# Kernel optimization log

Hardware: AMD Instinct MI355X
Metric: run time of the kernel (lower is better)

## Reference

```python
import jax, jax.numpy as jnp
import numpy as np

DIM = 16
HEADS = 2
EPS = 1e-5


def _layer_norm(x, g, b):
    m = x.mean(-1, keepdims=True)
    v = ((x - m) ** 2).mean(-1, keepdims=True)
    return (x - m) * jax.lax.rsqrt(v + EPS) * g + b


def setup_inputs() -> dict:
    key = jax.random.key(0)
    ks = jax.random.split(key, 8)
    B, Lq, Lk, D = 4, 2048, 2048, DIM
    xavier = float(np.sqrt(6.0 / (D + D)))  # xavier_uniform bound for square Linear
    inp = {
        "query": jax.random.normal(ks[0], (B, Lq, D), jnp.float32),
        "key": jax.random.normal(ks[1], (B, Lk, D), jnp.float32),
        "value": jax.random.normal(ks[2], (B, Lk, D), jnp.float32),
        "w": jax.random.normal(ks[3], (B, HEADS, Lq, Lk), jnp.float32) * 0.1,
        "mask": jnp.zeros((B, HEADS, Lq, Lk), jnp.float32),
        # LayerNorm params (q, k, v)
        "ln_qg": jnp.ones((D,), jnp.float32), "ln_qb": jnp.zeros((D,), jnp.float32),
        "ln_kg": jnp.ones((D,), jnp.float32), "ln_kb": jnp.zeros((D,), jnp.float32),
        "ln_vg": jnp.ones((D,), jnp.float32), "ln_vb": jnp.zeros((D,), jnp.float32),
        # Linear projections, torch layout [out, in]
        "Wq": jax.random.uniform(ks[4], (D, D), jnp.float32, -xavier, xavier),
        "bq": jnp.zeros((D,), jnp.float32),
        "Wk": jax.random.uniform(ks[5], (D, D), jnp.float32, -xavier, xavier),
        "bk": jnp.zeros((D,), jnp.float32),
        "Wv": jax.random.uniform(ks[6], (D, D), jnp.float32, -xavier, xavier),
        "bv": jnp.zeros((D,), jnp.float32),
        "Wo": jax.random.normal(ks[7], (D, D), jnp.float32) * (1.0 / np.sqrt(D)),
        "bo": jnp.zeros((D,), jnp.float32),
    }
    return inp


def reference(query, key, value, w, mask,
              ln_qg, ln_qb, ln_kg, ln_kb, ln_vg, ln_vb,
              Wq, bq, Wk, bk, Wv, bv, Wo, bo):
    B, Lq, D = query.shape
    H = HEADS
    dh = D // H
    q = _layer_norm(query, ln_qg, ln_qb)
    k = _layer_norm(key, ln_kg, ln_kb)
    v = _layer_norm(value, ln_vg, ln_vb)
    q0 = q  # residual is post-LayerNorm query
    # torch Linear: x @ W.T + b ; split heads -> [B, H, L, dh]
    Q = (q @ Wq.T + bq).reshape(B, Lq, H, dh).transpose(0, 2, 1, 3)
    K = (k @ Wk.T + bk).reshape(B, -1, H, dh).transpose(0, 2, 1, 3)
    V = (v @ Wv.T + bv).reshape(B, -1, H, dh).transpose(0, 2, 1, 3)
    Q = Q / (dh ** 0.5)
    scores = jnp.einsum('bhqd,bhkd->bhqk', Q, K) + w
    scores = scores - scores.max(axis=-1, keepdims=True)
    scores = scores + mask
    attn = jax.nn.softmax(scores, axis=-1)  # dropout is identity in eval
    ctx = jnp.einsum('bhqk,bhkd->bhqd', attn, V)
    ctx = ctx.transpose(0, 2, 1, 3).reshape(B, Lq, D)
    out = ctx @ Wo.T + bo + q0
    return out, attn
```

## Files before the change

kernel.cpp:

```cpp
#include <hip/hip_runtime.h>
#include <math.h>

#define BATCH 4
#define LQ 2048
#define LK 2048
#define DIM 16
#define HEADS 2
#define DH 8
#define EPS 1e-5f

typedef float fvec4 __attribute__((ext_vector_type(4)));

__global__ __launch_bounds__(256) void ln_proj3_kernel(
    const float* __restrict__ xq, const float* __restrict__ xk,
    const float* __restrict__ xv,
    const float* __restrict__ gq, const float* __restrict__ bq_ln,
    const float* __restrict__ gk, const float* __restrict__ bk_ln,
    const float* __restrict__ gv, const float* __restrict__ bv_ln,
    const float* __restrict__ Wq, const float* __restrict__ bq,
    const float* __restrict__ Wk, const float* __restrict__ bk,
    const float* __restrict__ Wv, const float* __restrict__ bv,
    float* __restrict__ Qb, float* __restrict__ Kb, float* __restrict__ Vb,
    float* __restrict__ q0)
{
    const int gid = blockIdx.x * blockDim.x + threadIdx.x;
    const int which = gid >> 13;
    const int r     = gid & 8191;

    const float* x; const float* g; const float* bl;
    const float* W; const float* bb; float* outp; float scale;
    if (which == 0)      { x = xq; g = gq; bl = bq_ln; W = Wq; bb = bq; outp = Qb; scale = 0.35355339059327373f; }
    else if (which == 1) { x = xk; g = gk; bl = bk_ln; W = Wk; bb = bk; outp = Kb; scale = 1.0f; }
    else                 { x = xv; g = gv; bl = bv_ln; W = Wv; bb = bv; outp = Vb; scale = 1.0f; }

    float xv16[16];
    const float4* xp = (const float4*)(x + (size_t)r * 16);
#pragma unroll
    for (int i = 0; i < 4; ++i) {
        float4 t = xp[i];
        xv16[4*i+0] = t.x; xv16[4*i+1] = t.y; xv16[4*i+2] = t.z; xv16[4*i+3] = t.w;
    }
    float m = 0.f;
#pragma unroll
    for (int i = 0; i < 16; ++i) m += xv16[i];
    m *= (1.f / 16.f);
    float var = 0.f;
#pragma unroll
    for (int i = 0; i < 16; ++i) { float d = xv16[i] - m; var += d * d; }
    var *= (1.f / 16.f);
    float rs = rsqrtf(var + EPS);

    float xn[16];
#pragma unroll
    for (int i = 0; i < 16; ++i) xn[i] = (xv16[i] - m) * rs * g[i] + bl[i];

    if (which == 0) {
        float4* op = (float4*)(q0 + (size_t)r * 16);
#pragma unroll
        for (int i = 0; i < 4; ++i) {
            float4 t; t.x = xn[4*i+0]; t.y = xn[4*i+1]; t.z = xn[4*i+2]; t.w = xn[4*i+3];
            op[i] = t;
        }
    }

    const int b = r >> 11;
    const int l = r & 2047;
#pragma unroll
    for (int j = 0; j < 16; ++j) {
        float acc = bb[j];
#pragma unroll
        for (int i = 0; i < 16; ++i) acc += xn[i] * W[j * 16 + i];
        acc *= scale;
        int h = j >> 3, d = j & 7;
        outp[((((size_t)b * HEADS + h) * 2048) + l) * DH + d] = acc;
    }
}

__device__ __forceinline__ float wave_sum(float v) {
#pragma unroll
    for (int off = 32; off > 0; off >>= 1) v += __shfl_xor(v, off);
    return v;
}

__global__ __launch_bounds__(512, 2) void attn_kernel(
    const float* __restrict__ Q,
    const float* __restrict__ K,
    const float* __restrict__ V,
    const float* __restrict__ w,
    const float* __restrict__ mask,
    float* __restrict__ attn_out,
    float* __restrict__ ctx)
{
    __shared__ float Ks[8][1024];
    __shared__ float Vs[8][1024];

    const int t    = threadIdx.x;
    const int lane = t & 63;
    const int wid  = t >> 6;
    const int bh   = blockIdx.x >> 8;
    const int qbase= (blockIdx.x & 255) << 3;
    const int q    = qbase + wid;
    const int rowid= (bh << 11) + q;
    const int h    = bh & (HEADS - 1);
    const int b    = bh >> 1;

    const float* Qrow = Q + (size_t)rowid * DH;
    float qv[8];
#pragma unroll
    for (int i = 0; i < 8; ++i) qv[i] = Qrow[i];

    const fvec4* Kg = (const fvec4*)(K + (size_t)bh * LK * DH);
    const fvec4* Vg = (const fvec4*)(V + (size_t)bh * LK * DH);
    const float* wrow = w    + (size_t)rowid * LK;
    const float* mrow = mask + (size_t)rowid * LK;

    fvec4 ebuf[8];
    float sum = 0.f;
    float cd[8] = {0,0,0,0,0,0,0,0};

#pragma unroll
    for (int chunk = 0; chunk < 2; ++chunk) {
        if (chunk) __syncthreads();
        {
            const int gbase = chunk << 10;
#pragma unroll
            for (int rr = 0; rr < 2; ++rr) {
                const int c = t + (rr << 9);
                fvec4 k0 = Kg[(size_t)(gbase + c) * 2 + 0];
                fvec4 k1 = Kg[(size_t)(gbase + c) * 2 + 1];
                fvec4 v0 = Vg[(size_t)(gbase + c) * 2 + 0];
                fvec4 v1 = Vg[(size_t)(gbase + c) * 2 + 1];
                Ks[0][c] = k0.x; Ks[1][c] = k0.y; Ks[2][c] = k0.z; Ks[3][c] = k0.w;
                Ks[4][c] = k1.x; Ks[5][c] = k1.y; Ks[6][c] = k1.z; Ks[7][c] = k1.w;
                Vs[0][c] = v0.x; Vs[1][c] = v0.y; Vs[2][c] = v0.z; Vs[3][c] = v0.w;
                Vs[4][c] = v1.x; Vs[5][c] = v1.y; Vs[6][c] = v1.z; Vs[7][c] = v1.w;
            }
        }
        __syncthreads();
#pragma unroll
        for (int i = 0; i < 4; ++i) {
            const int cbase = (i << 8) + (lane << 2);
            const int col   = (chunk << 10) + cbase;
            fvec4 wv = __builtin_nontemporal_load((const fvec4*)(wrow + col));
            fvec4 mv = __builtin_nontemporal_load((const fvec4*)(mrow + col));
            fvec4 s = wv + mv;
#pragma unroll
            for (int d = 0; d < 8; ++d) {
                fvec4 k4 = *(const fvec4*)&Ks[d][cbase];
                s += qv[d] * k4;
            }
            fvec4 e;
            e.x = __expf(s.x); e.y = __expf(s.y); e.z = __expf(s.z); e.w = __expf(s.w);
            ebuf[(chunk << 2) + i] = e;
            sum += e.x + e.y + e.z + e.w;
#pragma unroll
            for (int d = 0; d < 8; ++d) {
                fvec4 v4 = *(const fvec4*)&Vs[d][cbase];
                cd[d] += e.x * v4.x + e.y * v4.y + e.z * v4.z + e.w * v4.w;
            }
        }
    }

    sum = wave_sum(sum);
    const float inv = 1.f / sum;

    float* arow = attn_out + (size_t)rowid * LK;
#pragma unroll
    for (int j = 0; j < 8; ++j) {
        const int col = ((j >> 2) << 10) + ((j & 3) << 8) + (lane << 2);
        __builtin_nontemporal_store(ebuf[j] * inv, (fvec4*)(arow + col));
    }

#pragma unroll
    for (int d = 0; d < 8; ++d) cd[d] = wave_sum(cd[d]) * inv;
    if (lane == 0) {
        float* cp = ctx + ((((size_t)b * LQ + q) * HEADS) + h) * DH;
        fvec4 t0; t0.x = cd[0]; t0.y = cd[1]; t0.z = cd[2]; t0.w = cd[3];
        fvec4 t1; t1.x = cd[4]; t1.y = cd[5]; t1.z = cd[6]; t1.w = cd[7];
        ((fvec4*)cp)[0] = t0;
        ((fvec4*)cp)[1] = t1;
    }
}

__global__ __launch_bounds__(256) void out_kernel(
    const float* __restrict__ ctx,
    const float* __restrict__ Wo,
    const float* __restrict__ bo,
    const float* __restrict__ q0,
    float* __restrict__ out, int n)
{
    int gid = blockIdx.x * blockDim.x + threadIdx.x;
    if (gid >= n) return;
    int row = gid >> 4, j = gid & 15;
    const float* c = ctx + (size_t)row * 16;
    float acc = bo[j];
#pragma unroll
    for (int i = 0; i < 16; ++i) acc += c[i] * Wo[j * 16 + i];
    out[gid] = acc + q0[gid];
}

extern "C" void kernel_launch(void* const* d_in, const int* in_sizes, int n_in,
                              void* d_out, int out_size, void* d_ws, size_t ws_size,
                              hipStream_t stream) {
    const float* query = (const float*)d_in[0];
    const float* key_  = (const float*)d_in[1];
    const float* value = (const float*)d_in[2];
    const float* w     = (const float*)d_in[3];
    const float* mask  = (const float*)d_in[4];
    const float* ln_qg = (const float*)d_in[5];
    const float* ln_qb = (const float*)d_in[6];
    const float* ln_kg = (const float*)d_in[7];
    const float* ln_kb = (const float*)d_in[8];
    const float* ln_vg = (const float*)d_in[9];
    const float* ln_vb = (const float*)d_in[10];
    const float* Wq = (const float*)d_in[11];
    const float* bq = (const float*)d_in[12];
    const float* Wk = (const float*)d_in[13];
    const float* bk = (const float*)d_in[14];
    const float* Wv = (const float*)d_in[15];
    const float* bv = (const float*)d_in[16];
    const float* Wo = (const float*)d_in[17];
    const float* bo = (const float*)d_in[18];

    float* out  = (float*)d_out;
    float* attn = out + (size_t)BATCH * LQ * DIM;

    const size_t NE = (size_t)BATCH * LQ * DIM;
    float* ws  = (float*)d_ws;
    float* Qb  = ws;
    float* Kb  = Qb + NE;
    float* Vb  = Kb + NE;
    float* q0  = Vb + NE;
    float* ctx = q0 + NE;

    ln_proj3_kernel<<<(3 * 8192) / 256, 256, 0, stream>>>(
        query, key_, value,
        ln_qg, ln_qb, ln_kg, ln_kb, ln_vg, ln_vb,
        Wq, bq, Wk, bk, Wv, bv,
        Qb, Kb, Vb, q0);

    attn_kernel<<<BATCH * HEADS * LQ / 8, 512, 0, stream>>>(
        Qb, Kb, Vb, w, mask, attn, ctx);

    out_kernel<<<((int)NE + 255) / 256, 256, 0, stream>>>(
        ctx, Wo, bo, q0, out, (int)NE);
}
```

Baseline: 95.30 us.

## Keep K/V slices in registers and split key columns across waves

The attention kernel now gives each wave a fixed 256-key slice, with K and V for that slice held in registers. Each wave loops over the block's 8 query rows, prefetching the next row's w, mask and Q. Partial exp sums and context vectors are reduced within each wave by shuffles, then across waves through small shared arrays, and exp values are staged in LDS so each wave can normalise and write its own row. This drops the per-block K/V LDS transpose and the two-phase barrier loop, but adds a per-row shuffle reduction of nine values and a larger LDS exp buffer.

```diff
diff --git a/kernel.cpp b/kernel.cpp
--- a/kernel.cpp
+++ b/kernel.cpp
@@ -76,12 +76,6 @@
     }
 }
 
-__device__ __forceinline__ float wave_sum(float v) {
-#pragma unroll
-    for (int off = 32; off > 0; off >>= 1) v += __shfl_xor(v, off);
-    return v;
-}
-
 __global__ __launch_bounds__(512, 2) void attn_kernel(
     const float* __restrict__ Q,
     const float* __restrict__ K,
@@ -91,94 +85,96 @@
     float* __restrict__ attn_out,
     float* __restrict__ ctx)
 {
-    __shared__ float Ks[8][1024];
-    __shared__ float Vs[8][1024];
+    __shared__ fvec4 eS4[8][512];
+    __shared__ __align__(16) float credS[8][8][8];
+    __shared__ __align__(16) float psumS[8][8];
 
     const int t    = threadIdx.x;
     const int lane = t & 63;
     const int wid  = t >> 6;
     const int bh   = blockIdx.x >> 8;
     const int qbase= (blockIdx.x & 255) << 3;
-    const int q    = qbase + wid;
-    const int rowid= (bh << 11) + q;
     const int h    = bh & (HEADS - 1);
     const int b    = bh >> 1;
-
-    const float* Qrow = Q + (size_t)rowid * DH;
-    float qv[8];
-#pragma unroll
-    for (int i = 0; i < 8; ++i) qv[i] = Qrow[i];
+    const int c0   = (wid << 8) + (lane << 2);
 
     const fvec4* Kg = (const fvec4*)(K + (size_t)bh * LK * DH);
     const fvec4* Vg = (const fvec4*)(V + (size_t)bh * LK * DH);
-    const float* wrow = w    + (size_t)rowid * LK;
-    const float* mrow = mask + (size_t)rowid * LK;
-
-    fvec4 ebuf[8];
-    float sum = 0.f;
-    float cd[8] = {0,0,0,0,0,0,0,0};
-
-#pragma unroll
-    for (int chunk = 0; chunk < 2; ++chunk) {
-        if (chunk) __syncthreads();
-        {
-            const int gbase = chunk << 10;
-#pragma unroll
-            for (int rr = 0; rr < 2; ++rr) {
-                const int c = t + (rr << 9);
-                fvec4 k0 = Kg[(size_t)(gbase + c) * 2 + 0];
-                fvec4 k1 = Kg[(size_t)(gbase + c) * 2 + 1];
-                fvec4 v0 = Vg[(size_t)(gbase + c) * 2 + 0];
-                fvec4 v1 = Vg[(size_t)(gbase + c) * 2 + 1];
-                Ks[0][c] = k0.x; Ks[1][c] = k0.y; Ks[2][c] = k0.z; Ks[3][c] = k0.w;
-                Ks[4][c] = k1.x; Ks[5][c] = k1.y; Ks[6][c] = k1.z; Ks[7][c] = k1.w;
-                Vs[0][c] = v0.x; Vs[1][c] = v0.y; Vs[2][c] = v0.z; Vs[3][c] = v0.w;
-                Vs[4][c] = v1.x; Vs[5][c] = v1.y; Vs[6][c] = v1.z; Vs[7][c] = v1.w;
-            }
-        }
-        __syncthreads();
-#pragma unroll
-        for (int i = 0; i < 4; ++i) {
-            const int cbase = (i << 8) + (lane << 2);
-            const int col   = (chunk << 10) + cbase;
-            fvec4 wv = __builtin_nontemporal_load((const fvec4*)(wrow + col));
-            fvec4 mv = __builtin_nontemporal_load((const fvec4*)(mrow + col));
-            fvec4 s = wv + mv;
-#pragma unroll
-            for (int d = 0; d < 8; ++d) {
-                fvec4 k4 = *(const fvec4*)&Ks[d][cbase];
-                s += qv[d] * k4;
-            }
-            fvec4 e;
-            e.x = __expf(s.x); e.y = __expf(s.y); e.z = __expf(s.z); e.w = __expf(s.w);
-            ebuf[(chunk << 2) + i] = e;
-            sum += e.x + e.y + e.z + e.w;
-#pragma unroll
-            for (int d = 0; d < 8; ++d) {
-                fvec4 v4 = *(const fvec4*)&Vs[d][cbase];
-                cd[d] += e.x * v4.x + e.y * v4.y + e.z * v4.z + e.w * v4.w;
-            }
-        }
-    }
-
-    sum = wave_sum(sum);
-    const float inv = 1.f / sum;
-
-    float* arow = attn_out + (size_t)rowid * LK;
+    fvec4 klo[4], khi[4], vlo[4], vhi[4];
+#pragma unroll
+    for (int j = 0; j < 4; ++j) {
+        klo[j] = Kg[(size_t)(c0 + j) * 2 + 0];
+        khi[j] = Kg[(size_t)(c0 + j) * 2 + 1];
+        vlo[j] = Vg[(size_t)(c0 + j) * 2 + 0];
+        vhi[j] = Vg[(size_t)(c0 + j) * 2 + 1];
+    }
+
+    const float* wrow = w    + (((size_t)bh << 11) + qbase) * LK + c0;
+    const float* mrow = mask + (((size_t)bh << 11) + qbase) * LK + c0;
+    const fvec4* Qp   = (const fvec4*)(Q + (((size_t)bh << 11) + qbase) * DH);
+
+    fvec4 wv = __builtin_nontemporal_load((const fvec4*)wrow);
+    fvec4 mv = __builtin_nontemporal_load((const fvec4*)mrow);
+    fvec4 qlo = Qp[0], qhi = Qp[1];
+
+#pragma unroll
+    for (int r = 0; r < 8; ++r) {
+        fvec4 wn, mn, qnlo, qnhi;
+        if (r < 7) {
+            wn = __builtin_nontemporal_load((const fvec4*)(wrow + (size_t)(r + 1) * LK));
+            mn = __builtin_nontemporal_load((const fvec4*)(mrow + (size_t)(r + 1) * LK));
+            qnlo = Qp[2 * (r + 1)]; qnhi = Qp[2 * (r + 1) + 1];
+        }
+        fvec4 s = wv + mv;
+#pragma unroll
+        for (int j = 0; j < 4; ++j) {
+            s[j] += qlo.x * klo[j].x + qlo.y * klo[j].y + qlo.z * klo[j].z + qlo.w * klo[j].w
+                  + qhi.x * khi[j].x + qhi.y * khi[j].y + qhi.z * khi[j].z + qhi.w * khi[j].w;
+        }
+        fvec4 e;
+        e.x = __expf(s.x); e.y = __expf(s.y); e.z = __expf(s.z); e.w = __expf(s.w);
+        eS4[r][(wid << 6) + lane] = e;
+        float ps = e.x + e.y + e.z + e.w;
+        fvec4 cl = e.x * vlo[0] + e.y * vlo[1] + e.z * vlo[2] + e.w * vlo[3];
+        fvec4 ch = e.x * vhi[0] + e.y * vhi[1] + e.z * vhi[2] + e.w * vhi[3];
+#pragma unroll
+        for (int off = 32; off > 0; off >>= 1) {
+            ps   += __shfl_xor(ps, off);
+            cl.x += __shfl_xor(cl.x, off); cl.y += __shfl_xor(cl.y, off);
+            cl.z += __shfl_xor(cl.z, off); cl.w += __shfl_xor(cl.w, off);
+            ch.x += __shfl_xor(ch.x, off); ch.y += __shfl_xor(ch.y, off);
+            ch.z += __shfl_xor(ch.z, off); ch.w += __shfl_xor(ch.w, off);
+        }
+        if (lane == 0) {
+            psumS[r][wid] = ps;
+            *(fvec4*)&credS[r][wid][0] = cl;
+            *(fvec4*)&credS[r][wid][4] = ch;
+        }
+        wv = wn; mv = mn; qlo = qnlo; qhi = qnhi;
+    }
+
+    __syncthreads();
+
+    const int q = qbase + wid;
+    const size_t rowid = ((size_t)bh << 11) + q;
+    float rsum = 0.f;
+#pragma unroll
+    for (int j = 0; j < 8; ++j) rsum += psumS[wid][j];
+    const float inv = 1.f / rsum;
+
+    float* arow = attn_out + rowid * LK;
 #pragma unroll
     for (int j = 0; j < 8; ++j) {
-        const int col = ((j >> 2) << 10) + ((j & 3) << 8) + (lane << 2);
-        __builtin_nontemporal_store(ebuf[j] * inv, (fvec4*)(arow + col));
-    }
-
-#pragma unroll
-    for (int d = 0; d < 8; ++d) cd[d] = wave_sum(cd[d]) * inv;
-    if (lane == 0) {
-        float* cp = ctx + ((((size_t)b * LQ + q) * HEADS) + h) * DH;
-        fvec4 t0; t0.x = cd[0]; t0.y = cd[1]; t0.z = cd[2]; t0.w = cd[3];
-        fvec4 t1; t1.x = cd[4]; t1.y = cd[5]; t1.z = cd[6]; t1.w = cd[7];
-        ((fvec4*)cp)[0] = t0;
-        ((fvec4*)cp)[1] = t1;
+        const int ci = (j << 6) + lane;
+        fvec4 ev = eS4[wid][ci] * inv;
+        __builtin_nontemporal_store(ev, (fvec4*)(arow + (ci << 2)));
+    }
+
+    if (lane < 8) {
+        float acc = 0.f;
+#pragma unroll
+        for (int j = 0; j < 8; ++j) acc += credS[wid][j][lane];
+        ctx[((((size_t)b * LQ + q) * HEADS) + h) * DH + lane] = acc * inv;
     }
 }
 
```

Result: slower. 112.6 us (+18.1%).

## Store K/V in shared memory as packed bf16 pairs to fit whole sequence

Applied to the files above, without the earlier changes.

K and V tiles are rounded to bf16 and packed two dimensions per 32-bit word. This halves shared memory, so the full 2048-key sequence fits in one load phase with a single barrier instead of two chunked phases. It trades extra pack/unpack ALU work and reduced precision in the scores and context for fewer barriers and fewer LDS reads. Global traffic for w/mask/attn is unchanged, and that traffic likely dominates.

```diff
diff --git a/kernel.cpp b/kernel.cpp
--- a/kernel.cpp
+++ b/kernel.cpp
@@ -10,6 +10,22 @@
 #define EPS 1e-5f
 
 typedef float fvec4 __attribute__((ext_vector_type(4)));
+typedef unsigned int uvec4 __attribute__((ext_vector_type(4)));
+typedef unsigned int uvec2 __attribute__((ext_vector_type(2)));
+
+__device__ __forceinline__ unsigned pack_bf16(float lo, float hi) {
+    union { float f; unsigned u; } a, b;
+    a.f = lo; b.f = hi;
+    unsigned ua = (a.u + 0x7fffu + ((a.u >> 16) & 1u)) >> 16;
+    unsigned ub = (b.u + 0x7fffu + ((b.u >> 16) & 1u)) & 0xffff0000u;
+    return ua | ub;
+}
+__device__ __forceinline__ float bf_lo(unsigned u) {
+    union { unsigned u; float f; } c; c.u = u << 16; return c.f;
+}
+__device__ __forceinline__ float bf_hi(unsigned u) {
+    union { unsigned u; float f; } c; c.u = u & 0xffff0000u; return c.f;
+}
 
 __global__ __launch_bounds__(256) void ln_proj3_kernel(
     const float* __restrict__ xq, const float* __restrict__ xk,
@@ -91,8 +107,8 @@
     float* __restrict__ attn_out,
     float* __restrict__ ctx)
 {
-    __shared__ float Ks[8][1024];
-    __shared__ float Vs[8][1024];
+    __shared__ unsigned Kp[4][2048];
+    __shared__ unsigned Vp[4][2048];
 
     const int t    = threadIdx.x;
     const int lane = t & 63;
@@ -104,60 +120,80 @@
     const int h    = bh & (HEADS - 1);
     const int b    = bh >> 1;
 
+    {
+        const fvec4* Kg = (const fvec4*)(K + (size_t)bh * LK * DH);
+        const fvec4* Vg = (const fvec4*)(V + (size_t)bh * LK * DH);
+#pragma unroll
+        for (int half = 0; half < 2; ++half) {
+            const int c = 2 * t + (half << 10);
+            fvec4 kA0 = Kg[(size_t)c * 2 + 0],     kA1 = Kg[(size_t)c * 2 + 1];
+            fvec4 kB0 = Kg[(size_t)(c + 1) * 2 + 0], kB1 = Kg[(size_t)(c + 1) * 2 + 1];
+            fvec4 vA0 = Vg[(size_t)c * 2 + 0],     vA1 = Vg[(size_t)c * 2 + 1];
+            fvec4 vB0 = Vg[(size_t)(c + 1) * 2 + 0], vB1 = Vg[(size_t)(c + 1) * 2 + 1];
+            uvec2 u;
+            u.x = pack_bf16(kA0.x, kA0.y); u.y = pack_bf16(kB0.x, kB0.y);
+            *(uvec2*)&Kp[0][c] = u;
+            u.x = pack_bf16(kA0.z, kA0.w); u.y = pack_bf16(kB0.z, kB0.w);
+            *(uvec2*)&Kp[1][c] = u;
+            u.x = pack_bf16(kA1.x, kA1.y); u.y = pack_bf16(kB1.x, kB1.y);
+            *(uvec2*)&Kp[2][c] = u;
+            u.x = pack_bf16(kA1.z, kA1.w); u.y = pack_bf16(kB1.z, kB1.w);
+            *(uvec2*)&Kp[3][c] = u;
+            u.x = pack_bf16(vA0.x, vA0.y); u.y = pack_bf16(vB0.x, vB0.y);
+            *(uvec2*)&Vp[0][c] = u;
+            u.x = pack_bf16(vA0.z, vA0.w); u.y = pack_bf16(vB0.z, vB0.w);
+            *(uvec2*)&Vp[1][c] = u;
+            u.x = pack_bf16(vA1.x, vA1.y); u.y = pack_bf16(vB1.x, vB1.y);
+            *(uvec2*)&Vp[2][c] = u;
+            u.x = pack_bf16(vA1.z, vA1.w); u.y = pack_bf16(vB1.z, vB1.w);
+            *(uvec2*)&Vp[3][c] = u;
+        }
+    }
+
     const float* Qrow = Q + (size_t)rowid * DH;
     float qv[8];
 #pragma unroll
     for (int i = 0; i < 8; ++i) qv[i] = Qrow[i];
 
-    const fvec4* Kg = (const fvec4*)(K + (size_t)bh * LK * DH);
-    const fvec4* Vg = (const fvec4*)(V + (size_t)bh * LK * DH);
     const float* wrow = w    + (size_t)rowid * LK;
     const float* mrow = mask + (size_t)rowid * LK;
+
+    __syncthreads();
 
     fvec4 ebuf[8];
     float sum = 0.f;
     float cd[8] = {0,0,0,0,0,0,0,0};
 
 #pragma unroll
-    for (int chunk = 0; chunk < 2; ++chunk) {
-        if (chunk) __syncthreads();
-        {
-            const int gbase = chunk << 10;
-#pragma unroll
-            for (int rr = 0; rr < 2; ++rr) {
-                const int c = t + (rr << 9);
-                fvec4 k0 = Kg[(size_t)(gbase + c) * 2 + 0];
-                fvec4 k1 = Kg[(size_t)(gbase + c) * 2 + 1];
-                fvec4 v0 = Vg[(size_t)(gbase + c) * 2 + 0];
-                fvec4 v1 = Vg[(size_t)(gbase + c) * 2 + 1];
-                Ks[0][c] = k0.x; Ks[1][c] = k0.y; Ks[2][c] = k0.z; Ks[3][c] = k0.w;
-                Ks[4][c] = k1.x; Ks[5][c] = k1.y; Ks[6][c] = k1.z; Ks[7][c] = k1.w;
-                Vs[0][c] = v0.x; Vs[1][c] = v0.y; Vs[2][c] = v0.z; Vs[3][c] = v0.w;
-                Vs[4][c] = v1.x; Vs[5][c] = v1.y; Vs[6][c] = v1.z; Vs[7][c] = v1.w;
+    for (int i = 0; i < 8; ++i) {
+        const int cb = (i << 8) + (lane << 2);
+        fvec4 wv = __builtin_nontemporal_load((const fvec4*)(wrow + cb));
+        fvec4 mv = __builtin_nontemporal_load((const fvec4*)(mrow + cb));
+        fvec4 s = wv + mv;
+#pragma unroll
+        for (int p = 0; p < 4; ++p) {
+            uvec4 kk = *(const uvec4*)&Kp[p][cb];
+            const float qa = qv[2 * p], qb = qv[2 * p + 1];
+#pragma unroll
+            for (int j = 0; j < 4; ++j) {
+                s[j] += qa * bf_lo(kk[j]) + qb * bf_hi(kk[j]);
             }
         }
-        __syncthreads();
-#pragma unroll
-        for (int i = 0; i < 4; ++i) {
-            const int cbase = (i << 8) + (lane << 2);
-            const int col   = (chunk << 10) + cbase;
-            fvec4 wv = __builtin_nontemporal_load((const fvec4*)(wrow + col));
-            fvec4 mv = __builtin_nontemporal_load((const fvec4*)(mrow + col));
-            fvec4 s = wv + mv;
-#pragma unroll
-            for (int d = 0; d < 8; ++d) {
-                fvec4 k4 = *(const fvec4*)&Ks[d][cbase];
-                s += qv[d] * k4;
+        fvec4 e;
+        e.x = __expf(s.x); e.y = __expf(s.y); e.z = __expf(s.z); e.w = __expf(s.w);
+        ebuf[i] = e;
+        sum += e.x + e.y + e.z + e.w;
+#pragma unroll
+        for (int p = 0; p < 4; ++p) {
+            uvec4 vv = *(const uvec4*)&Vp[p][cb];
+            float a0 = 0.f, a1 = 0.f;
+#pragma unroll
+            for (int j = 0; j < 4; ++j) {
+                a0 += e[j] * bf_lo(vv[j]);
+                a1 += e[j] * bf_hi(vv[j]);
             }
-            fvec4 e;
-            e.x = __expf(s.x); e.y = __expf(s.y); e.z = __expf(s.z); e.w = __expf(s.w);
-            ebuf[(chunk << 2) + i] = e;
-            sum += e.x + e.y + e.z + e.w;
-#pragma unroll
-            for (int d = 0; d < 8; ++d) {
-                fvec4 v4 = *(const fvec4*)&Vs[d][cbase];
-                cd[d] += e.x * v4.x + e.y * v4.y + e.z * v4.z + e.w * v4.w;
-            }
+            cd[2 * p]     += a0;
+            cd[2 * p + 1] += a1;
         }
     }
 
@@ -166,9 +202,9 @@
 
     float* arow = attn_out + (size_t)rowid * LK;
 #pragma unroll
-    for (int j = 0; j < 8; ++j) {
-        const int col = ((j >> 2) << 10) + ((j & 3) << 8) + (lane << 2);
-        __builtin_nontemporal_store(ebuf[j] * inv, (fvec4*)(arow + col));
+    for (int i = 0; i < 8; ++i) {
+        const int cb = (i << 8) + (lane << 2);
+        __builtin_nontemporal_store(ebuf[i] * inv, (fvec4*)(arow + cb));
     }
 
 #pragma unroll
```

New measurement: 112.8 us. 1.18x slower.
